# Kernel optimization log

Hardware: AMD Instinct MI355X
Metric: run time of the kernel (lower is better)

## Reference

```python
import jax, jax.numpy as jnp
import numpy as np

ALPHA = 0.5  # LeakyReLU negative slope


def setup_inputs() -> dict:
    key = jax.random.key(0)
    k1, k2, k3, k4, k5 = jax.random.split(key, 5)
    B, N, S, SO, K = 16, 2048, 12, 12, 32
    return {
        "fushed_features": jax.random.normal(k1, (B, N, 64), dtype=jnp.float32),
        "input_data": jax.random.normal(k2, (B, N, S), dtype=jnp.float32),
        "W": jax.random.normal(k3, (S, SO), dtype=jnp.float32) * (1.414 / np.sqrt(S)),
        "a": jax.random.normal(k4, (2 * SO, 1), dtype=jnp.float32) * 0.3,
        "idx": jax.random.randint(k5, (B, N, K), 0, N, dtype=jnp.int32),
    }


def reference(fushed_features, input_data, W, a, idx):
    # input_data: (B, N, S); W: (S, SO); a: (2*SO, 1); idx: (B, N, K)
    B, N, S = input_data.shape
    SO = W.shape[1]
    wh = input_data @ W  # (B, N, SO)
    # concat([wh_i, wh_j]) @ a  ==  wh_i @ a[:SO] + wh_j @ a[SO:]  (exact same math,
    # avoids materializing the (B,N,N,2*SO) concat the torch code builds)
    e_src = wh @ a[:SO, 0]  # (B, N)
    e_dst = wh @ a[SO:, 0]  # (B, N)
    scores = jax.nn.leaky_relu(e_src[:, :, None] + e_dst[:, None, :], negative_slope=ALPHA)  # (B,N,N)
    att = jnp.take_along_axis(scores, idx, axis=2)  # (B, N, K) gather top-k neighbor scores
    att = jax.nn.softmax(att, axis=-1)  # softmax over the K neighbors
    # gather neighbor time series: (B, N, K, S)
    neigh = input_data[jnp.arange(B)[:, None, None], idx]
    out = att[..., None] * neigh  # (B, N, K, S)
    return out
```

## Files before the change

kernel.cpp:

```cpp
#include <hip/hip_runtime.h>


#define GAT_N 2048
#define GAT_ALPHA 0.5f
#define PPBLK 128
#define THREADS 1024

__global__ __launch_bounds__(THREADS, 1) void gat_lds(
    const float* __restrict__ x,
    const float* __restrict__ W,
    const float* __restrict__ a,
    const int*   __restrict__ idx,
    float*       __restrict__ out)
{
    __shared__ float rows[GAT_N * 12];
    __shared__ float edt[GAT_N];
    __shared__ float es_loc[PPBLK];
    __shared__ float wvec[24];

    const int tid   = threadIdx.x;
    const int b     = blockIdx.x >> 4;
    const int blk16 = blockIdx.x & 15;

    if (tid < 24) {
        const int s = tid % 12;
        const float* av = a + (tid < 12 ? 0 : 12);
        float acc = 0.f;
        #pragma unroll
        for (int t = 0; t < 12; ++t) acc += W[s * 12 + t] * av[t];
        wvec[tid] = acc;
    }

    {
        const float4* g4 = (const float4*)(x + (size_t)b * GAT_N * 12);
        float4* l4 = (float4*)rows;
        #pragma unroll
        for (int r = 0; r < 6; ++r) l4[tid + THREADS * r] = g4[tid + THREADS * r];
    }
    __syncthreads();

    #pragma unroll
    for (int c = 0; c < 2; ++c) {
        const int n = tid + THREADS * c;
        const float* row = rows + n * 12;
        float acc = 0.f;
        #pragma unroll
        for (int t = 0; t < 12; ++t) acc += row[t] * wvec[12 + t];
        edt[n] = acc;
    }
    if (tid < PPBLK) {
        const float* row = rows + (blk16 * PPBLK + tid) * 12;
        float acc = 0.f;
        #pragma unroll
        for (int t = 0; t < 12; ++t) acc += row[t] * wvec[t];
        es_loc[tid] = acc;
    }
    __syncthreads();

    const int slot = tid >> 5;
    const int k    = tid & 31;
    const int pairG0 = (b << 11) + blk16 * PPBLK + slot;

    int jv[4];
    #pragma unroll
    for (int t = 0; t < 4; ++t)
        jv[t] = idx[(size_t)(pairG0 + 32 * t) * 32 + k];

    float ex[4], sum[4];
    #pragma unroll
    for (int t = 0; t < 4; ++t) {
        float e = es_loc[slot + 32 * t] + edt[jv[t]];
        e = e > 0.f ? e : GAT_ALPHA * e;
        ex[t] = __expf(fminf(e, 80.f));
        sum[t] = ex[t];
    }
    #pragma unroll
    for (int off = 16; off; off >>= 1) {
        #pragma unroll
        for (int t = 0; t < 4; ++t) sum[t] += __shfl_xor(sum[t], off, 32);
    }
    float att[4];
    #pragma unroll
    for (int t = 0; t < 4; ++t) att[t] = ex[t] / sum[t];

    #pragma unroll
    for (int t = 0; t < 4; ++t) {
        float4* o4 = (float4*)out + (size_t)(pairG0 + 32 * t) * 96;
        #pragma unroll
        for (int r = 0; r < 3; ++r) {
            const int f  = r * 32 + k;
            const int kk = f / 3;
            const int q  = f - 3 * kk;
            const float attk = __shfl(att[t], kk, 32);
            const int   jk   = __shfl(jv[t],  kk, 32);
            const float4 v = *(const float4*)(rows + jk * 12 + 4 * q);
            o4[f] = make_float4(attk * v.x, attk * v.y, attk * v.z, attk * v.w);
        }
    }
}

__global__ __launch_bounds__(256) void gat_fused(
    const float* __restrict__ x, const float* __restrict__ W,
    const float* __restrict__ a, const int* __restrict__ idx,
    float* __restrict__ out)
{
    __shared__ float wvec[24];
    __shared__ float stage[8 * 384];
    const int tid = threadIdx.x;

    if (tid < 24) {
        const int s = tid % 12;
        const float* av = a + (tid < 12 ? 0 : 12);
        float acc = 0.f;
        #pragma unroll
        for (int t = 0; t < 12; ++t) acc += W[s * 12 + t] * av[t];
        wvec[tid] = acc;
    }
    __syncthreads();

    const int p    = tid >> 5;
    const int pair = blockIdx.x * 8 + p;
    const int k    = tid & 31;

    const float4* rowi = (const float4*)(x + (size_t)pair * 12);
    const float4 i0 = rowi[0], i1 = rowi[1], i2 = rowi[2];
    const float e_src =
        i0.x*wvec[0] + i0.y*wvec[1] + i0.z*wvec[2]  + i0.w*wvec[3] +
        i1.x*wvec[4] + i1.y*wvec[5] + i1.z*wvec[6]  + i1.w*wvec[7] +
        i2.x*wvec[8] + i2.y*wvec[9] + i2.z*wvec[10] + i2.w*wvec[11];

    const int j   = idx[(size_t)pair * 32 + k];
    const int nbr = (pair & ~(GAT_N - 1)) + j;
    const float4* rowj = (const float4*)(x + (size_t)nbr * 12);
    const float4 n0 = rowj[0], n1 = rowj[1], n2 = rowj[2];
    const float e_dst =
        n0.x*wvec[12] + n0.y*wvec[13] + n0.z*wvec[14] + n0.w*wvec[15] +
        n1.x*wvec[16] + n1.y*wvec[17] + n1.z*wvec[18] + n1.w*wvec[19] +
        n2.x*wvec[20] + n2.y*wvec[21] + n2.z*wvec[22] + n2.w*wvec[23];

    float sc = e_src + e_dst;
    sc = sc > 0.f ? sc : GAT_ALPHA * sc;
    float m = sc;
    #pragma unroll
    for (int off = 16; off; off >>= 1) m = fmaxf(m, __shfl_xor(m, off, 32));
    const float ex = __expf(sc - m);
    float sum = ex;
    #pragma unroll
    for (int off = 16; off; off >>= 1) sum += __shfl_xor(sum, off, 32);
    const float att = ex / sum;

    float4* st = (float4*)(stage + p * 384 + k * 12);
    st[0] = make_float4(att * n0.x, att * n0.y, att * n0.z, att * n0.w);
    st[1] = make_float4(att * n1.x, att * n1.y, att * n1.z, att * n1.w);
    st[2] = make_float4(att * n2.x, att * n2.y, att * n2.z, att * n2.w);
    __syncthreads();

    const float4* sm4 = (const float4*)stage;
    float4* o4 = (float4*)(out + (size_t)blockIdx.x * 8 * 384);
    #pragma unroll
    for (int r = 0; r < 3; ++r) o4[tid + 256 * r] = sm4[tid + 256 * r];
}

extern "C" void kernel_launch(void* const* d_in, const int* in_sizes, int n_in,
                              void* d_out, int out_size, void* d_ws, size_t ws_size,
                              hipStream_t stream) {
    const float* x   = (const float*)d_in[1];
    const float* W   = (const float*)d_in[2];
    const float* a   = (const float*)d_in[3];
    const int*   idx = (const int*)d_in[4];
    float* out = (float*)d_out;

    const int pairs = in_sizes[1] / 12;

    if ((pairs & (GAT_N - 1)) == 0) {
        gat_lds<<<pairs / PPBLK, THREADS, 0, stream>>>(x, W, a, idx, out);
    } else {
        gat_fused<<<pairs / 8, 256, 0, stream>>>(x, W, a, idx, out);
    }
}
```

Before: 85.54 us.

## Compute attention projections from registers and drop one block barrier

```diff
diff --git a/kernel.cpp b/kernel.cpp
--- a/kernel.cpp
+++ b/kernel.cpp
@@ -16,49 +16,13 @@
     __shared__ float rows[GAT_N * 12];
     __shared__ float edt[GAT_N];
     __shared__ float es_loc[PPBLK];
-    __shared__ float wvec[24];
 
     const int tid   = threadIdx.x;
     const int b     = blockIdx.x >> 4;
     const int blk16 = blockIdx.x & 15;
 
-    if (tid < 24) {
-        const int s = tid % 12;
-        const float* av = a + (tid < 12 ? 0 : 12);
-        float acc = 0.f;
-        #pragma unroll
-        for (int t = 0; t < 12; ++t) acc += W[s * 12 + t] * av[t];
-        wvec[tid] = acc;
-    }
-
-    {
-        const float4* g4 = (const float4*)(x + (size_t)b * GAT_N * 12);
-        float4* l4 = (float4*)rows;
-        #pragma unroll
-        for (int r = 0; r < 6; ++r) l4[tid + THREADS * r] = g4[tid + THREADS * r];
-    }
-    __syncthreads();
-
-    #pragma unroll
-    for (int c = 0; c < 2; ++c) {
-        const int n = tid + THREADS * c;
-        const float* row = rows + n * 12;
-        float acc = 0.f;
-        #pragma unroll
-        for (int t = 0; t < 12; ++t) acc += row[t] * wvec[12 + t];
-        edt[n] = acc;
-    }
-    if (tid < PPBLK) {
-        const float* row = rows + (blk16 * PPBLK + tid) * 12;
-        float acc = 0.f;
-        #pragma unroll
-        for (int t = 0; t < 12; ++t) acc += row[t] * wvec[t];
-        es_loc[tid] = acc;
-    }
-    __syncthreads();
-
-    const int slot = tid >> 5;
-    const int k    = tid & 31;
+    const int slot   = tid >> 5;
+    const int k      = tid & 31;
     const int pairG0 = (b << 11) + blk16 * PPBLK + slot;
 
     int jv[4];
@@ -66,12 +30,64 @@
     for (int t = 0; t < 4; ++t)
         jv[t] = idx[(size_t)(pairG0 + 32 * t) * 32 + k];
 
+    const float4* gp = (const float4*)(x + (size_t)b * GAT_N * 12 + (size_t)tid * 24);
+    const float4 v0 = gp[0], v1 = gp[1], v2 = gp[2];
+    const float4 v3 = gp[3], v4 = gp[4], v5 = gp[5];
+
+    float acc;
+    {
+        const int l     = tid & 63;
+        const int idx24 = l % 24;
+        const int s     = idx24 % 12;
+        const float* av = a + (idx24 < 12 ? 0 : 12);
+        acc = 0.f;
+        #pragma unroll
+        for (int t = 0; t < 12; ++t) acc += W[s * 12 + t] * av[t];
+    }
+    float wvd[12];
+    #pragma unroll
+    for (int s = 0; s < 12; ++s) wvd[s] = __shfl(acc, 12 + s, 64);
+
+    const float ed0 =
+        v0.x*wvd[0] + v0.y*wvd[1] + v0.z*wvd[2]  + v0.w*wvd[3] +
+        v1.x*wvd[4] + v1.y*wvd[5] + v1.z*wvd[6]  + v1.w*wvd[7] +
+        v2.x*wvd[8] + v2.y*wvd[9] + v2.z*wvd[10] + v2.w*wvd[11];
+    const float ed1 =
+        v3.x*wvd[0] + v3.y*wvd[1] + v3.z*wvd[2]  + v3.w*wvd[3] +
+        v4.x*wvd[4] + v4.y*wvd[5] + v4.z*wvd[6]  + v4.w*wvd[7] +
+        v5.x*wvd[8] + v5.y*wvd[9] + v5.z*wvd[10] + v5.w*wvd[11];
+
+    if ((tid >> 6) == blk16) {
+        float wvs[12];
+        #pragma unroll
+        for (int s = 0; s < 12; ++s) wvs[s] = __shfl(acc, s, 64);
+        const float es0 =
+            v0.x*wvs[0] + v0.y*wvs[1] + v0.z*wvs[2]  + v0.w*wvs[3] +
+            v1.x*wvs[4] + v1.y*wvs[5] + v1.z*wvs[6]  + v1.w*wvs[7] +
+            v2.x*wvs[8] + v2.y*wvs[9] + v2.z*wvs[10] + v2.w*wvs[11];
+        const float es1 =
+            v3.x*wvs[0] + v3.y*wvs[1] + v3.z*wvs[2]  + v3.w*wvs[3] +
+            v4.x*wvs[4] + v4.y*wvs[5] + v4.z*wvs[6]  + v4.w*wvs[7] +
+            v5.x*wvs[8] + v5.y*wvs[9] + v5.z*wvs[10] + v5.w*wvs[11];
+        const int local2 = 2 * tid - blk16 * PPBLK;
+        es_loc[local2]     = es0;
+        es_loc[local2 + 1] = es1;
+    }
+
+    {
+        float4* lp = (float4*)(rows + tid * 24);
+        lp[0] = v0; lp[1] = v1; lp[2] = v2;
+        lp[3] = v3; lp[4] = v4; lp[5] = v5;
+        *(float2*)(edt + 2 * tid) = make_float2(ed0, ed1);
+    }
+    __syncthreads();
+
     float ex[4], sum[4];
     #pragma unroll
     for (int t = 0; t < 4; ++t) {
         float e = es_loc[slot + 32 * t] + edt[jv[t]];
         e = e > 0.f ? e : GAT_ALPHA * e;
-        ex[t] = __expf(fminf(e, 80.f));
+        ex[t]  = __expf(fminf(e, 80.f));
         sum[t] = ex[t];
     }
     #pragma unroll
```

After: 85.56 us (median of 2 runs). Within noise of the previous version (+0.0%).
